# Kernel optimization log

Measured on AMD Instinct MI355X. Metric: run time of the kernel, lower is better.

## Reference

```python
import jax, jax.numpy as jnp
import numpy as np

D_MODEL = 256
D_INNER = 512
D_STATE = 16
DT_RANK = 16
D_CONV = 4
N_LAYERS = 2
EPS = 1e-5
SEQ_LEN = 16384
IN_DIM = 32
OUT_DIM = 1


def _layernorm(x, g, b):
    m = jnp.mean(x, axis=-1, keepdims=True)
    v = jnp.mean((x - m) ** 2, axis=-1, keepdims=True)
    return (x - m) * jax.lax.rsqrt(v + EPS) * g + b


def _rmsnorm(x, w):
    return x * jax.lax.rsqrt(jnp.mean(x * x, axis=-1, keepdims=True) + EPS) * w


def _selective_scan(x, delta, A, B, C, D):
    # x, delta: (B,L,ED); A: (ED,N); B,C: (B,L,N); D: (ED,)
    dA = jnp.exp(delta[..., None] * A)                    # (B,L,ED,N)
    dBx = (delta * x)[..., None] * B[:, :, None, :]       # (B,L,ED,N)

    def comb(l, r):
        al, bl = l
        ar, br = r
        return (al * ar, bl * ar + br)

    _, hs = jax.lax.associative_scan(comb, (dA, dBx), axis=1)  # (B,L,ED,N)
    y = jnp.einsum('blen,bln->ble', hs, C) + x * D
    return y


def _mamba_block(u, rms_w, inW, convW, convB, xpW, dtW, dtB, A_log, Dp, outW):
    h = _rmsnorm(u, rms_w)
    xz = h @ inW                                   # (B,L,2*ED)
    xin, z = jnp.split(xz, 2, axis=-1)
    # depthwise causal conv1d over time
    xc = jax.lax.conv_general_dilated(
        jnp.transpose(xin, (0, 2, 1)), convW,
        window_strides=(1,), padding=[(D_CONV - 1, 0)],
        feature_group_count=D_INNER,
        dimension_numbers=('NCH', 'OIH', 'NCH')) + convB[None, :, None]
    xs = jax.nn.silu(jnp.transpose(xc, (0, 2, 1)))  # (B,L,ED)
    dbc = xs @ xpW                                  # (B,L,dt_rank+2N)
    delta = jax.nn.softplus(dbc[..., :DT_RANK] @ dtW + dtB)
    Bm = dbc[..., DT_RANK:DT_RANK + D_STATE]
    Cm = dbc[..., DT_RANK + D_STATE:]
    y = _selective_scan(xs, delta, -jnp.exp(A_log), Bm, Cm, Dp)
    out = (y * jax.nn.silu(z)) @ outW
    return u + out  # residual


def _forward(x, W_in, b_in, ln1_g, ln1_b,
             rms_w, inW, convW, convB, xpW, dtW, dtB, A_log, Dp, outW,
             ln2_g, ln2_b, W1, b1, ln3_g, ln3_b, W2, b2):
    # input_proj (dropout = identity in eval)
    h = jax.nn.gelu(_layernorm(x[0] @ W_in + b_in, ln1_g, ln1_b))
    h = h[None]  # (1,L,D)
    for i in range(N_LAYERS):
        h = _mamba_block(h, rms_w[i], inW[i], convW[i], convB[i], xpW[i],
                         dtW[i], dtB[i], A_log[i], Dp[i], outW[i])
    # output_proj
    h = _layernorm(h, ln2_g, ln2_b)
    h = jax.nn.gelu(h @ W1 + b1)
    h = _layernorm(h, ln3_g, ln3_b)
    h = jnp.tanh(h @ W2 + b2)
    return h.reshape(-1)


def setup_inputs() -> dict:
    key = jax.random.key(0)
    ks = jax.random.split(key, 16)
    s = 0.02
    A = jnp.tile(jnp.arange(1, D_STATE + 1, dtype=jnp.float32)[None, :], (D_INNER, 1))
    return {
        'x': jax.random.normal(ks[0], (1, SEQ_LEN, IN_DIM), jnp.float32),
        'W_in': s * jax.random.normal(ks[1], (IN_DIM, D_MODEL), jnp.float32),
        'b_in': jnp.zeros((D_MODEL,), jnp.float32),
        'ln1_g': jnp.ones((D_MODEL,), jnp.float32),
        'ln1_b': jnp.zeros((D_MODEL,), jnp.float32),
        'rms_w': jnp.ones((N_LAYERS, D_MODEL), jnp.float32),
        'inW': s * jax.random.normal(ks[2], (N_LAYERS, D_MODEL, 2 * D_INNER), jnp.float32),
        'convW': s * jax.random.normal(ks[3], (N_LAYERS, D_INNER, 1, D_CONV), jnp.float32),
        'convB': jnp.zeros((N_LAYERS, D_INNER), jnp.float32),
        'xpW': s * jax.random.normal(ks[4], (N_LAYERS, D_INNER, DT_RANK + 2 * D_STATE), jnp.float32),
        'dtW': s * jax.random.normal(ks[5], (N_LAYERS, DT_RANK, D_INNER), jnp.float32),
        'dtB': 0.1 * jax.random.normal(ks[6], (N_LAYERS, D_INNER), jnp.float32),
        'A_log': jnp.tile(jnp.log(A)[None], (N_LAYERS, 1, 1)),
        'Dp': jnp.ones((N_LAYERS, D_INNER), jnp.float32),
        'outW': s * jax.random.normal(ks[7], (N_LAYERS, D_INNER, D_MODEL), jnp.float32),
        'ln2_g': jnp.ones((D_MODEL,), jnp.float32),
        'ln2_b': jnp.zeros((D_MODEL,), jnp.float32),
        'W1': s * jax.random.normal(ks[8], (D_MODEL, D_MODEL // 2), jnp.float32),
        'b1': jnp.zeros((D_MODEL // 2,), jnp.float32),
        'ln3_g': jnp.ones((D_MODEL // 2,), jnp.float32),
        'ln3_b': jnp.zeros((D_MODEL // 2,), jnp.float32),
        'W2': s * jax.random.normal(ks[9], (D_MODEL // 2, OUT_DIM), jnp.float32),
        'b2': jnp.zeros((OUT_DIM,), jnp.float32),
    }


def reference(x, W_in, b_in, ln1_g, ln1_b, rms_w, inW, convW, convB, xpW,
              dtW, dtB, A_log, Dp, outW, ln2_g, ln2_b, W1, b1, ln3_g, ln3_b,
              W2, b2):
    return _forward(x, W_in, b_in, ln1_g, ln1_b, rms_w, inW, convW, convB,
                    xpW, dtW, dtB, A_log, Dp, outW, ln2_g, ln2_b, W1, b1,
                    ln3_g, ln3_b, W2, b2)
```

## Files before the change

kernel.cpp:

```cpp
#include <hip/hip_runtime.h>
#include <hip/hip_bf16.h>
#include <math.h>

#define L_SEQ 16384
#define DM 256
#define DI 512
#define DS 16
#define NCH 512
#define CHL 32
#define CLB 16

typedef __attribute__((ext_vector_type(8))) short short8v;
typedef __attribute__((ext_vector_type(4))) float f32x4;

__device__ __forceinline__ float tanh_fast(float x){
  float xc = fminf(x, 15.f);
  float t = __expf(2.f*xc);
  return (t-1.f)/(t+1.f);
}
__device__ __forceinline__ float gelu_f(float x){
  float x3 = x*x*x;
  return 0.5f*x*(1.0f + tanh_fast(0.7978845608028654f*(x + 0.044715f*x3)));
}
__device__ __forceinline__ float silu_f(float x){
  return x / (1.0f + __expf(-x));
}
__device__ __forceinline__ float softplus_f(float x){
  return fmaxf(x,0.0f) + __logf(1.0f + __expf(-fabsf(x)));
}
__device__ __forceinline__ float bf2f(unsigned short u){
  return __uint_as_float(((unsigned int)u)<<16);
}
__device__ __forceinline__ void gload16(const void* g, void* l){
  __builtin_amdgcn_global_load_lds((const __attribute__((address_space(1))) void*)g,
                                   (__attribute__((address_space(3))) void*)l, 16, 0, 0);
}

__device__ __forceinline__ void powers16(float r, float* dA){
  float r2 = r*r;
  float r4 = r2*r2;
  float r8 = r4*r4;
  dA[0]=r;        dA[1]=r2;       dA[2]=r2*r;     dA[3]=r4;
  dA[4]=r4*r;     dA[5]=r4*r2;    dA[6]=r4*dA[2]; dA[7]=r8;
  dA[8]=r8*r;     dA[9]=r8*r2;    dA[10]=r8*dA[2];dA[11]=r8*r4;
  dA[12]=r8*dA[4];dA[13]=r8*dA[5];dA[14]=r8*dA[6];dA[15]=r8*r8;
}

__global__ void k_prep(const float* __restrict__ inW, const float* __restrict__ rmsw,
                       const float* __restrict__ outW, const float* __restrict__ W1,
                       const float* __restrict__ xpW, const float* __restrict__ dtW,
                       __hip_bfloat16* __restrict__ inWt, __hip_bfloat16* __restrict__ outWt,
                       __hip_bfloat16* __restrict__ W1t, __hip_bfloat16* __restrict__ Wdbc_t,
                       float* __restrict__ rowsq1){
  int idx = blockIdx.x*256 + threadIdx.x;
  if(idx < 524288){
    int layer = idx >> 18;
    int r = idx & 262143;
    int n = r >> 8, k = r & 255;
    inWt[idx] = __float2bfloat16(inW[layer*262144 + k*1024 + n] * rmsw[layer*256+k]);
  } else if(idx < 786432){
    int j = idx - 524288;
    int layer = j >> 17;
    int r = j & 131071;
    int n = r >> 9, k = r & 511;
    outWt[j] = __float2bfloat16(outW[layer*131072 + k*256 + n]);
  } else if(idx < 819200){
    int j = idx - 786432;
    int n = j >> 8, k = j & 255;
    W1t[j] = __float2bfloat16(W1[k*128 + n]);
  } else if(idx < 1474560){
    int j = idx - 819200;
    int layer = j / 327680;
    int r = j % 327680;
    int n = r >> 9, k = r & 511;
    const float* xp = xpW + layer*512*48;
    float v;
    if(n < 512){
      const float* dt = dtW + layer*16*512;
      float s = 0.f;
#pragma unroll
      for(int q=0;q<16;q++) s = fmaf(xp[k*48+q], dt[q*512+n], s);
      v = s;
    } else if(n < 544){
      v = xp[k*48 + 16 + (n-512)];
    } else v = 0.f;
    Wdbc_t[j] = __float2bfloat16(v);
  } else if(idx < 1490944){
    rowsq1[idx - 1474560] = 0.f;
  }
}

__global__ __launch_bounds__(256) void k_input(const float* __restrict__ x,
                        const float* __restrict__ Win, const float* __restrict__ bin,
                        const float* __restrict__ g, const float* __restrict__ b,
                        __hip_bfloat16* __restrict__ u, float* __restrict__ rowsq){
  int wv = threadIdx.x>>6, lane = threadIdx.x&63;
  int r = blockIdx.x*4 + wv;
  int c0 = lane*4;
  float acc[4];
  { float4 bv = *(const float4*)&bin[c0];
    acc[0]=bv.x; acc[1]=bv.y; acc[2]=bv.z; acc[3]=bv.w; }
#pragma unroll
  for(int k=0;k<32;k++){
    float xk = x[r*32+k];
    float4 wv4 = *(const float4*)&Win[k*DM+c0];
    acc[0]=fmaf(xk,wv4.x,acc[0]); acc[1]=fmaf(xk,wv4.y,acc[1]);
    acc[2]=fmaf(xk,wv4.z,acc[2]); acc[3]=fmaf(xk,wv4.w,acc[3]);
  }
  float s = (acc[0]+acc[1])+(acc[2]+acc[3]);
  float sq = acc[0]*acc[0]+acc[1]*acc[1]+acc[2]*acc[2]+acc[3]*acc[3];
#pragma unroll
  for(int o=32;o;o>>=1){ s += __shfl_xor(s,o); sq += __shfl_xor(sq,o); }
  float mean = s*(1.0f/DM);
  float var = sq*(1.0f/DM) - mean*mean;
  float rs = rsqrtf(var+1e-5f);
  float4 gv = *(const float4*)&g[c0];
  float4 bv = *(const float4*)&b[c0];
  float go[4];
  go[0] = gelu_f((acc[0]-mean)*rs*gv.x+bv.x);
  go[1] = gelu_f((acc[1]-mean)*rs*gv.y+bv.y);
  go[2] = gelu_f((acc[2]-mean)*rs*gv.z+bv.z);
  go[3] = gelu_f((acc[3]-mean)*rs*gv.w+bv.w);
  float ssq = go[0]*go[0]+go[1]*go[1]+go[2]*go[2]+go[3]*go[3];
#pragma unroll
  for(int o=32;o;o>>=1) ssq += __shfl_xor(ssq,o);
  if(lane==0) rowsq[r] = ssq;
  __hip_bfloat16 ob[4] = {__float2bfloat16(go[0]),__float2bfloat16(go[1]),
                          __float2bfloat16(go[2]),__float2bfloat16(go[3])};
  *(uint2*)&u[r*DM+c0] = *(uint2*)ob;
}

__global__ __launch_bounds__(256) void k_ln(const __hip_bfloat16* __restrict__ u,
                     const float* __restrict__ g, const float* __restrict__ b,
                     __hip_bfloat16* __restrict__ o){
  int wv = threadIdx.x>>6, lane = threadIdx.x&63;
  int r = blockIdx.x*4 + wv;
  int c0 = lane*4;
  ushort4 uv = *(const ushort4*)&u[r*DM+c0];
  float v[4] = {bf2f(uv.x), bf2f(uv.y), bf2f(uv.z), bf2f(uv.w)};
  float s = (v[0]+v[1])+(v[2]+v[3]);
  float sq = v[0]*v[0]+v[1]*v[1]+v[2]*v[2]+v[3]*v[3];
#pragma unroll
  for(int o2=32;o2;o2>>=1){ s += __shfl_xor(s,o2); sq += __shfl_xor(sq,o2); }
  float mean = s*(1.0f/DM);
  float var = sq*(1.0f/DM) - mean*mean;
  float rs = rsqrtf(var+1e-5f);
  float4 gv = *(const float4*)&g[c0];
  float4 bv = *(const float4*)&b[c0];
  __hip_bfloat16 ob[4] = {
    __float2bfloat16((v[0]-mean)*rs*gv.x+bv.x),
    __float2bfloat16((v[1]-mean)*rs*gv.y+bv.y),
    __float2bfloat16((v[2]-mean)*rs*gv.z+bv.z),
    __float2bfloat16((v[3]-mean)*rs*gv.w+bv.w)};
  *(uint2*)&o[r*DM+c0] = *(uint2*)ob;
}

template<int EPI, typename OT>
__global__ __launch_bounds__(512) void k_mgemm(const __hip_bfloat16* __restrict__ A,
    const __hip_bfloat16* __restrict__ Wt, const float* __restrict__ bias,
    const OT* __restrict__ R, OT* __restrict__ C, float* __restrict__ C2,
    float* __restrict__ rowsq, int M, int K, int ldc, int Nout){
  __shared__ char lds[66560];
  float* Ob = (float*)lds;
  int t = threadIdx.x, lane = t&63, wave = t>>6;
  int gx = gridDim.x;
  int f = blockIdx.y*gx + blockIdx.x;
  int s = f >> 3;
  int sy = s/gx;
  int yb = (f&7)*(gridDim.y>>3) + sy;
  int xb = s - sy*gx;
  int m0 = yb*128, n0 = xb*128;
  int wm = (wave>>1)*32, wn = (wave&1)*64;
  f32x4 acc[2][4] = {};
  int soff[2], srow[2], scol[2];
#pragma unroll
  for(int c=0;c<2;c++){
    int off = c*8192 + t*16;
    int row = off>>7;
    int sl  = ((off>>4)&7) ^ (row&7);
    soff[c]=off; srow[c]=row; scol[c]=sl*8;
  }
  int nk = K >> 6;
#pragma unroll
  for(int c=0;c<2;c++){
    gload16(&A [(m0+srow[c])*K + scol[c]], lds + soff[c]);
    gload16(&Wt[(n0+srow[c])*K + scol[c]], lds + 32768 + soff[c]);
  }
  for(int ki=0; ki<nk; ki++){
    int co = (ki & 1) ? 16384 : 0;
    if(ki+1 < nk){
      int no = co ^ 16384;
      int kt = (ki+1)<<6;
#pragma unroll
      for(int c=0;c<2;c++){
        gload16(&A [(m0+srow[c])*K + kt + scol[c]], lds + no + soff[c]);
        gload16(&Wt[(n0+srow[c])*K + kt + scol[c]], lds + 32768 + no + soff[c]);
      }
      asm volatile("s_waitcnt vmcnt(4)" ::: "memory");
    } else {
      asm volatile("s_waitcnt vmcnt(0)" ::: "memory");
    }
    __builtin_amdgcn_s_barrier();
    asm volatile("" ::: "memory");
    const short* As = (const short*)(lds + co);
    const short* Bs = (const short*)(lds + 32768 + co);
#pragma unroll
    for(int ks=0; ks<2; ks++){
      short8v a[2], b[4];
      int k8 = ks*4 + (lane>>4);
#pragma unroll
      for(int i=0;i<2;i++){
        int lr = wm + i*16 + (lane&15);
        a[i] = *(const short8v*)&As[lr*64 + (k8 ^ (lr&7))*8];
      }
#pragma unroll
      for(int j=0;j<4;j++){
        int lr = wn + j*16 + (lane&15);
        b[j] = *(const short8v*)&Bs[lr*64 + (k8 ^ (lr&7))*8];
      }
#pragma unroll
      for(int i=0;i<2;i++)
#pragma unroll
        for(int j=0;j<4;j++)
          acc[i][j] = __builtin_amdgcn_mfma_f32_16x16x32_bf16(a[i], b[j], acc[i][j], 0,0,0);
    }
    asm volatile("" ::: "memory");
    __builtin_amdgcn_s_barrier();
  }
#pragma unroll
  for(int h=0; h<2; h++){
    __syncthreads();
    if((wm>>6)==h){
      int base = wm & 63;
#pragma unroll
      for(int i=0;i<2;i++)
#pragma unroll
        for(int j=0;j<4;j++)
#pragma unroll
          for(int r=0;r<4;r++)
            Ob[(base + i*16 + (lane>>4)*4 + r)*132 + wn + j*16 + (lane&15)] = acc[i][j][r];
    }
    __syncthreads();
    float ssq_acc = 0.f;
#pragma unroll
    for(int v=0; v<4; v++){
      int fidx = (t*4+v)*4;
      int row = fidx>>7, col = fidx&127;
      if(col < Nout){
        float4 o = *(const float4*)&Ob[row*132 + col];
        int grow = m0 + h*64 + row, gcol = n0 + col;
        if(EPI==1 || EPI==5){
          if constexpr(sizeof(OT)==2){
            ushort4 rv = *(const ushort4*)&R[grow*ldc+gcol];
            o.x+=bf2f(rv.x); o.y+=bf2f(rv.y); o.z+=bf2f(rv.z); o.w+=bf2f(rv.w);
          } else {
            float4 rv = *(const float4*)&R[grow*ldc+gcol];
            o.x+=rv.x; o.y+=rv.y; o.z+=rv.z; o.w+=rv.w;
          }
          if(EPI==5) ssq_acc += o.x*o.x + o.y*o.y + o.z*o.z + o.w*o.w;
        }
        if(EPI==2){
          float4 bv = *(const float4*)&bias[gcol];
          o.x=gelu_f(o.x+bv.x); o.y=gelu_f(o.y+bv.y);
          o.z=gelu_f(o.z+bv.z); o.w=gelu_f(o.w+bv.w);
        }
        if(EPI==6){
          float rs = rsqrtf(rowsq[grow]*(1.0f/DM) + 1e-5f);
          o.x*=rs; o.y*=rs; o.z*=rs; o.w*=rs;
        }
        if(EPI==4){
          if(gcol < 512){
            float4 bv = *(const float4*)&bias[gcol];
            float4 so = {softplus_f(o.x+bv.x), softplus_f(o.y+bv.y),
                         softplus_f(o.z+bv.z), softplus_f(o.w+bv.w)};
            __hip_bfloat16 ob[4] = {__float2bfloat16(so.x),__float2bfloat16(so.y),
                                    __float2bfloat16(so.z),__float2bfloat16(so.w)};
            *(uint2*)&C[grow*ldc+gcol] = *(uint2*)ob;
          } else {
            *(float4*)&C2[grow*32 + (gcol-512)] = o;
          }
        } else {
          if constexpr(sizeof(OT)==2){
            __hip_bfloat16 ob[4] = {__float2bfloat16(o.x),__float2bfloat16(o.y),
                                    __float2bfloat16(o.z),__float2bfloat16(o.w)};
            *(uint2*)&C[grow*ldc+gcol] = *(uint2*)ob;
          } else {
            *(float4*)&C[grow*ldc+gcol] = o;
          }
        }
      }
    }
    if(EPI==5){
      ssq_acc += __shfl_xor(ssq_acc,1);
      ssq_acc += __shfl_xor(ssq_acc,2);
      ssq_acc += __shfl_xor(ssq_acc,4);
      if((t&7)==0) atomicAdd(&rowsq[m0 + h*64 + (t>>3)], ssq_acc);
    }
  }
}

__global__ __launch_bounds__(256) void k_conv(const __hip_bfloat16* __restrict__ xz,
                       const float* __restrict__ cw, const float* __restrict__ cb,
                       __hip_bfloat16* __restrict__ xs_bf){
  int idx = blockIdx.x*256 + threadIdx.x;
  int cg = idx & 127, lb = idx >> 7;
  int c4 = cg*4;
  int l0 = lb*CLB;
  float w[4][4], bias[4];
#pragma unroll
  for(int j=0;j<4;j++){
    float4 wv = *(const float4*)&cw[(c4+j)*4];
    w[j][0]=wv.x; w[j][1]=wv.y; w[j][2]=wv.z; w[j][3]=wv.w;
  }
  { float4 bv = *(const float4*)&cb[c4];
    bias[0]=bv.x; bias[1]=bv.y; bias[2]=bv.z; bias[3]=bv.w; }
  float xm0[4], xm1[4], xm2[4];
#pragma unroll
  for(int j=0;j<4;j++){ xm0[j]=0.f; xm1[j]=0.f; xm2[j]=0.f; }
  if(l0 >= 3){
    ushort4 r0 = *(const ushort4*)&xz[(l0-3)*1024 + c4];
    ushort4 r1 = *(const ushort4*)&xz[(l0-2)*1024 + c4];
    ushort4 r2 = *(const ushort4*)&xz[(l0-1)*1024 + c4];
    xm0[0]=bf2f(r0.x); xm0[1]=bf2f(r0.y); xm0[2]=bf2f(r0.z); xm0[3]=bf2f(r0.w);
    xm1[0]=bf2f(r1.x); xm1[1]=bf2f(r1.y); xm1[2]=bf2f(r1.z); xm1[3]=bf2f(r1.w);
    xm2[0]=bf2f(r2.x); xm2[1]=bf2f(r2.y); xm2[2]=bf2f(r2.z); xm2[3]=bf2f(r2.w);
  }
#pragma unroll 4
  for(int l=l0; l<l0+CLB; l++){
    ushort4 rc = *(const ushort4*)&xz[l*1024 + c4];
    float xc[4] = {bf2f(rc.x), bf2f(rc.y), bf2f(rc.z), bf2f(rc.w)};
    __hip_bfloat16 ob[4];
#pragma unroll
    for(int j=0;j<4;j++){
      float acc = bias[j];
      acc = fmaf(xm0[j], w[j][0], acc);
      acc = fmaf(xm1[j], w[j][1], acc);
      acc = fmaf(xm2[j], w[j][2], acc);
      acc = fmaf(xc[j],  w[j][3], acc);
      ob[j] = __float2bfloat16(silu_f(acc));
    }
    *(uint2*)&xs_bf[l*DI + c4] = *(uint2*)ob;
#pragma unroll
    for(int j=0;j<4;j++){ xm0[j]=xm1[j]; xm1[j]=xm2[j]; xm2[j]=xc[j]; }
  }
}

__global__ __launch_bounds__(256) void k_scan1(const __hip_bfloat16* __restrict__ delta,
                        const __hip_bfloat16* __restrict__ xs,
                        const float* __restrict__ dbc32, const float* __restrict__ A_log,
                        __hip_bfloat16* __restrict__ Atot, __hip_bfloat16* __restrict__ Btot){
  __shared__ float bcs[CHL*32];
  int t = threadIdx.x;
  int chunk = blockIdx.x >> 1;
  int e = ((blockIdx.x & 1) << 8) + t;
  int l0 = chunk*CHL;
  ((float4*)bcs)[t] = ((const float4*)&dbc32[l0*32])[t];
  float A[16];
  {
    const float4* al = (const float4*)&A_log[e*DS];
#pragma unroll
    for(int q=0;q<4;q++){
      float4 a = al[q];
      A[q*4+0] = -__expf(a.x); A[q*4+1] = -__expf(a.y);
      A[q*4+2] = -__expf(a.z); A[q*4+3] = -__expf(a.w);
    }
  }
  bool pf = true;
#pragma unroll
  for(int n=1;n<16;n++) pf = pf && (fabsf(A[n] - (n+1)*A[0]) <= 1e-4f*fabsf(A[n]));
  float carry[16], aprod[16];
#pragma unroll
  for(int n=0;n<16;n++){ carry[n]=0.f; aprod[n]=1.f; }
  __syncthreads();
  if(pf){
    float A0 = A[0];
#pragma unroll 2
    for(int li=0; li<CHL; li++){
      int l = l0 + li;
      float d  = bf2f(*(const unsigned short*)&delta[l*DI+e]);
      float xv = bf2f(*(const unsigned short*)&xs[l*DI+e]);
      float dxv = d*xv;
      const float4* bp = (const float4*)&bcs[li*32];
      float4 b0=bp[0], b1=bp[1], b2=bp[2], b3=bp[3];
      float B[16] = {b0.x,b0.y,b0.z,b0.w, b1.x,b1.y,b1.z,b1.w,
                     b2.x,b2.y,b2.z,b2.w, b3.x,b3.y,b3.z,b3.w};
      float r = __expf(d*A0);
      float dA[16]; powers16(r, dA);
#pragma unroll
      for(int n=0;n<16;n++){
        carry[n] = fmaf(carry[n], dA[n], dxv*B[n]);
        aprod[n] *= dA[n];
      }
    }
  } else {
#pragma unroll 2
    for(int li=0; li<CHL; li++){
      int l = l0 + li;
      float d  = bf2f(*(const unsigned short*)&delta[l*DI+e]);
      float xv = bf2f(*(const unsigned short*)&xs[l*DI+e]);
      float dxv = d*xv;
      const float4* bp = (const float4*)&bcs[li*32];
      float4 b0=bp[0], b1=bp[1], b2=bp[2], b3=bp[3];
      float B[16] = {b0.x,b0.y,b0.z,b0.w, b1.x,b1.y,b1.z,b1.w,
                     b2.x,b2.y,b2.z,b2.w, b3.x,b3.y,b3.z,b3.w};
#pragma unroll
      for(int n=0;n<16;n++){
        float dA = __expf(d*A[n]);
        carry[n] = fmaf(carry[n], dA, dxv*B[n]);
        aprod[n] *= dA;
      }
    }
  }
  __hip_bfloat16 apk[16], bpk[16];
#pragma unroll
  for(int n=0;n<16;n++){
    apk[n] = __float2bfloat16(aprod[n]);
    bpk[n] = __float2bfloat16(carry[n]);
  }
  uint4* ap = (uint4*)&Atot[chunk*8192 + e*DS];
  uint4* bp = (uint4*)&Btot[chunk*8192 + e*DS];
  ap[0] = ((const uint4*)apk)[0]; ap[1] = ((const uint4*)apk)[1];
  bp[0] = ((const uint4*)bpk)[0]; bp[1] = ((const uint4*)bpk)[1];
}

__global__ __launch_bounds__(64) void k_scan2(const __hip_bfloat16* __restrict__ Atot,
                        const __hip_bfloat16* __restrict__ Btot,
                        __hip_bfloat16* __restrict__ h0){
  int tg = blockIdx.x*64 + threadIdx.x;
  float carry = 0.f;
  for(int c0=0;c0<NCH;c0+=8){
    float a[8], b[8];
#pragma unroll
    for(int j=0;j<8;j++){
      a[j] = bf2f(*(const unsigned short*)&Atot[(c0+j)*8192+tg]);
      b[j] = bf2f(*(const unsigned short*)&Btot[(c0+j)*8192+tg]);
    }
#pragma unroll
    for(int j=0;j<8;j++){
      h0[(c0+j)*8192+tg] = __float2bfloat16(carry);
      carry = fmaf(carry, a[j], b[j]);
    }
  }
}

__global__ __launch_bounds__(256) void k_scan3(const __hip_bfloat16* __restrict__ delta,
                        const __hip_bfloat16* __restrict__ xs,
                        const float* __restrict__ dbc32, const float* __restrict__ A_log,
                        const float* __restrict__ Dp, const __hip_bfloat16* __restrict__ h0,
                        const __hip_bfloat16* __restrict__ xz, __hip_bfloat16* __restrict__ y){
  __shared__ float bcs[CHL*32];
  int t = threadIdx.x;
  int chunk = blockIdx.x >> 1;
  int e = ((blockIdx.x & 1) << 8) + t;
  int l0 = chunk*CHL;
  ((float4*)bcs)[t] = ((const float4*)&dbc32[l0*32])[t];
  float A[16];
  {
    const float4* al = (const float4*)&A_log[e*DS];
#pragma unroll
    for(int q=0;q<4;q++){
      float4 a = al[q];
      A[q*4+0] = -__expf(a.x); A[q*4+1] = -__expf(a.y);
      A[q*4+2] = -__expf(a.z); A[q*4+3] = -__expf(a.w);
    }
  }
  bool pf = true;
#pragma unroll
  for(int n=1;n<16;n++) pf = pf && (fabsf(A[n] - (n+1)*A[0]) <= 1e-4f*fabsf(A[n]));
  float carry[16];
  {
    uint4 h0a = ((const uint4*)&h0[chunk*8192 + e*DS])[0];
    uint4 h0b = ((const uint4*)&h0[chunk*8192 + e*DS])[1];
    const unsigned short* hp = (const unsigned short*)&h0a;
#pragma unroll
    for(int n=0;n<8;n++) carry[n] = bf2f(hp[n]);
    const unsigned short* hq = (const unsigned short*)&h0b;
#pragma unroll
    for(int n=0;n<8;n++) carry[8+n] = bf2f(hq[n]);
  }
  float Dv = Dp[e];
  __syncthreads();
  if(pf){
    float A0 = A[0];
#pragma unroll 2
    for(int li=0; li<CHL; li++){
      int l = l0 + li;
      float d  = bf2f(*(const unsigned short*)&delta[l*DI+e]);
      float xv = bf2f(*(const unsigned short*)&xs[l*DI+e]);
      float dxv = d*xv;
      const float4* bp = (const float4*)&bcs[li*32];
      float4 b0=bp[0], b1=bp[1], b2=bp[2], b3=bp[3];
      float4 c0=bp[4], c1=bp[5], c2=bp[6], c3=bp[7];
      float B[16] = {b0.x,b0.y,b0.z,b0.w, b1.x,b1.y,b1.z,b1.w,
                     b2.x,b2.y,b2.z,b2.w, b3.x,b3.y,b3.z,b3.w};
      float Cv[16] = {c0.x,c0.y,c0.z,c0.w, c1.x,c1.y,c1.z,c1.w,
                      c2.x,c2.y,c2.z,c2.w, c3.x,c3.y,c3.z,c3.w};
      float r = __expf(d*A0);
      float dA[16]; powers16(r, dA);
      float p[4] = {0.f,0.f,0.f,0.f};
#pragma unroll
      for(int n=0;n<16;n++){
        carry[n] = fmaf(carry[n], dA[n], dxv*B[n]);
        p[n&3] = fmaf(carry[n], Cv[n], p[n&3]);
      }
      float ps = (p[0]+p[1]) + (p[2]+p[3]);
      float z = bf2f(*(const unsigned short*)&xz[l*1024 + 512 + e]);
      y[l*DI+e] = __float2bfloat16(fmaf(xv, Dv, ps) * silu_f(z));
    }
  } else {
#pragma unroll 2
    for(int li=0; li<CHL; li++){
      int l = l0 + li;
      float d  = bf2f(*(const unsigned short*)&delta[l*DI+e]);
      float xv = bf2f(*(const unsigned short*)&xs[l*DI+e]);
      float dxv = d*xv;
      const float4* bp = (const float4*)&bcs[li*32];
      float4 b0=bp[0], b1=bp[1], b2=bp[2], b3=bp[3];
      float4 c0=bp[4], c1=bp[5], c2=bp[6], c3=bp[7];
      float B[16] = {b0.x,b0.y,b0.z,b0.w, b1.x,b1.y,b1.z,b1.w,
                     b2.x,b2.y,b2.z,b2.w, b3.x,b3.y,b3.z,b3.w};
      float Cv[16] = {c0.x,c0.y,c0.z,c0.w, c1.x,c1.y,c1.z,c1.w,
                      c2.x,c2.y,c2.z,c2.w, c3.x,c3.y,c3.z,c3.w};
      float p[4] = {0.f,0.f,0.f,0.f};
#pragma unroll
      for(int n=0;n<16;n++){
        float dA = __expf(d*A[n]);
        carry[n] = fmaf(carry[n], dA, dxv*B[n]);
        p[n&3] = fmaf(carry[n], Cv[n], p[n&3]);
      }
      float ps = (p[0]+p[1]) + (p[2]+p[3]);
      float z = bf2f(*(const unsigned short*)&xz[l*1024 + 512 + e]);
      y[l*DI+e] = __float2bfloat16(fmaf(xv, Dv, ps) * silu_f(z));
    }
  }
}

__global__ void k_final(const float* __restrict__ h2, const float* __restrict__ g,
                        const float* __restrict__ b, const float* __restrict__ W2,
                        const float* __restrict__ b2, float* __restrict__ out){
  int lane = threadIdx.x&63;
  int wv = threadIdx.x>>6;
  int r = blockIdx.x*4 + wv;
  float v0 = h2[r*128+lane], v1 = h2[r*128+64+lane];
  float s = v0+v1, sq = v0*v0+v1*v1;
#pragma unroll
  for(int o=32;o;o>>=1){ s += __shfl_xor(s,o); sq += __shfl_xor(sq,o); }
  float mean = s*(1.0f/128), var = sq*(1.0f/128) - mean*mean;
  float rs = rsqrtf(var+1e-5f);
  float n0 = (v0-mean)*rs*g[lane]+b[lane];
  float n1 = (v1-mean)*rs*g[lane+64]+b[lane+64];
  float d = n0*W2[lane] + n1*W2[lane+64];
#pragma unroll
  for(int o=32;o;o>>=1) d += __shfl_xor(d,o);
  if(lane==0) out[r] = tanhf(d + b2[0]);
}

extern "C" void kernel_launch(void* const* d_in, const int* in_sizes, int n_in,
                              void* d_out, int out_size, void* d_ws, size_t ws_size,
                              hipStream_t stream){
  const float* x    = (const float*)d_in[0];
  const float* Win  = (const float*)d_in[1];
  const float* bin  = (const float*)d_in[2];
  const float* ln1g = (const float*)d_in[3];
  const float* ln1b = (const float*)d_in[4];
  const float* rmsw = (const float*)d_in[5];
  const float* inW  = (const float*)d_in[6];
  const float* convW= (const float*)d_in[7];
  const float* convB= (const float*)d_in[8];
  const float* xpW  = (const float*)d_in[9];
  const float* dtW  = (const float*)d_in[10];
  const float* dtB  = (const float*)d_in[11];
  const float* A_log= (const float*)d_in[12];
  const float* Dp   = (const float*)d_in[13];
  const float* outW = (const float*)d_in[14];
  const float* ln2g = (const float*)d_in[15];
  const float* ln2b = (const float*)d_in[16];
  const float* W1   = (const float*)d_in[17];
  const float* b1   = (const float*)d_in[18];
  const float* ln3g = (const float*)d_in[19];
  const float* ln3b = (const float*)d_in[20];
  const float* W2   = (const float*)d_in[21];
  const float* b2   = (const float*)d_in[22];
  float* out = (float*)d_out;
  float* ws = (float*)d_ws;
  __hip_bfloat16* u_bf = (__hip_bfloat16*)ws;
  float* rowsq0 = ws + 4194304;
  float* rowsq1 = ws + 4210688;
  __hip_bfloat16* hn_bf = (__hip_bfloat16*)(ws + 4259840);
  __hip_bfloat16* xz_bf = (__hip_bfloat16*)(ws + 8388608);
  float* dbc32 = ws + 16777216;
  __hip_bfloat16* delta_bf = (__hip_bfloat16*)(ws + 17301504);
  __hip_bfloat16* y_bf  = (__hip_bfloat16*)(ws + 25690112);
  __hip_bfloat16* xs_bf = (__hip_bfloat16*)(ws + 29884416);
  __hip_bfloat16* Atot  = (__hip_bfloat16*)(ws + 34078720);
  __hip_bfloat16* Btot  = (__hip_bfloat16*)(ws + 36175872);
  __hip_bfloat16* h0    = Btot;
  float* h2    = ws;
  __hip_bfloat16* inWt   = (__hip_bfloat16*)(ws + 42467328);
  __hip_bfloat16* outWt  = (__hip_bfloat16*)(ws + 42729472);
  __hip_bfloat16* W1t    = (__hip_bfloat16*)(ws + 42860544);
  __hip_bfloat16* Wdbc_t = (__hip_bfloat16*)(ws + 42876928);

  k_prep<<<5824,256,0,stream>>>(inW, rmsw, outW, W1, xpW, dtW, inWt, outWt, W1t, Wdbc_t, rowsq1);
  k_input<<<L_SEQ/4,256,0,stream>>>(x,Win,bin,ln1g,ln1b,u_bf,rowsq0);
  for(int i=0;i<2;i++){
    float* rsq_in = (i==0) ? rowsq0 : rowsq1;
    k_mgemm<6,__hip_bfloat16><<<dim3(8, L_SEQ/128),512,0,stream>>>(
        u_bf, inWt+i*262144, nullptr, nullptr, xz_bf, nullptr, rsq_in, L_SEQ, DM, 1024, 1024);
    k_conv<<<(L_SEQ/CLB)*128/256,256,0,stream>>>(xz_bf, convW+i*DI*4, convB+i*DI, xs_bf);
    k_mgemm<4,__hip_bfloat16><<<dim3(5, L_SEQ/128),512,0,stream>>>(
        xs_bf, Wdbc_t+i*327680, dtB+i*DI, nullptr, delta_bf, dbc32, nullptr, L_SEQ, DI, 512, 544);
    k_scan1<<<NCH*2,256,0,stream>>>(delta_bf, xs_bf, dbc32, A_log+i*DI*DS, Atot, Btot);
    k_scan2<<<128,64,0,stream>>>(Atot, Btot, h0);
    k_scan3<<<NCH*2,256,0,stream>>>(delta_bf, xs_bf, dbc32, A_log+i*DI*DS, Dp+i*DI, h0, xz_bf, y_bf);
    if(i==0){
      k_mgemm<5,__hip_bfloat16><<<dim3(2, L_SEQ/128),512,0,stream>>>(
          y_bf, outWt, nullptr, u_bf, u_bf, nullptr, rowsq1, L_SEQ, DI, 256, 256);
    } else {
      k_mgemm<1,__hip_bfloat16><<<dim3(2, L_SEQ/128),512,0,stream>>>(
          y_bf, outWt+131072, nullptr, u_bf, u_bf, nullptr, nullptr, L_SEQ, DI, 256, 256);
    }
  }
  k_ln<<<L_SEQ/4,256,0,stream>>>(u_bf, ln2g, ln2b, hn_bf);
  k_mgemm<2,float><<<dim3(1, L_SEQ/128),512,0,stream>>>(
      hn_bf, W1t, b1, nullptr, h2, nullptr, nullptr, L_SEQ, DM, 128, 128);
  k_final<<<L_SEQ/4,256,0,stream>>>(h2, ln3g, ln3b, W2, b2, out);
}
```

Baseline: 357.7 us.

## Fold final LayerNorm into W1 GEMM and fuse output head into epilogue

The ln2 gamma is folded into W1, and the ln2 beta/bias terms are precomputed into a parameter vector. Row sums and sums of squares are accumulated atomically in the last out-projection epilogue, so the standalone LayerNorm kernel is removed. The W1 GEMM now reads the residual stream directly and applies mean/rstd, GELU, LN3, the W2 dot and tanh in its epilogue, which eliminates the k_ln and k_final launches and the h2/hn intermediates. The trade-offs are extra atomics and changed numerics: variance is computed from bf16-rounded sums, and the folded weights are quantized to bf16.

```diff
diff --git a/kernel.cpp b/kernel.cpp
--- a/kernel.cpp
+++ b/kernel.cpp
@@ -49,9 +49,14 @@
 __global__ void k_prep(const float* __restrict__ inW, const float* __restrict__ rmsw,
                        const float* __restrict__ outW, const float* __restrict__ W1,
                        const float* __restrict__ xpW, const float* __restrict__ dtW,
+                       const float* __restrict__ ln2g, const float* __restrict__ ln2b,
+                       const float* __restrict__ b1, const float* __restrict__ ln3g,
+                       const float* __restrict__ ln3b, const float* __restrict__ W2,
+                       const float* __restrict__ b2,
                        __hip_bfloat16* __restrict__ inWt, __hip_bfloat16* __restrict__ outWt,
                        __hip_bfloat16* __restrict__ W1t, __hip_bfloat16* __restrict__ Wdbc_t,
-                       float* __restrict__ rowsq1){
+                       float* __restrict__ rowsq1, float* __restrict__ rowsum2,
+                       float* __restrict__ rowsq2, float* __restrict__ pars){
   int idx = blockIdx.x*256 + threadIdx.x;
   if(idx < 524288){
     int layer = idx >> 18;
@@ -67,7 +72,7 @@
   } else if(idx < 819200){
     int j = idx - 786432;
     int n = j >> 8, k = j & 255;
-    W1t[j] = __float2bfloat16(W1[k*128 + n]);
+    W1t[j] = __float2bfloat16(W1[k*128 + n] * ln2g[k]);
   } else if(idx < 1474560){
     int j = idx - 819200;
     int layer = j / 327680;
@@ -87,6 +92,25 @@
     Wdbc_t[j] = __float2bfloat16(v);
   } else if(idx < 1490944){
     rowsq1[idx - 1474560] = 0.f;
+  } else if(idx < 1507328){
+    rowsum2[idx - 1490944] = 0.f;
+  } else if(idx < 1523712){
+    rowsq2[idx - 1507328] = 0.f;
+  } else if(idx < 1524353){
+    int j = idx - 1523712;
+    if(j < 128){
+      float s = 0.f;
+      for(int k=0;k<256;k++) s = fmaf(ln2g[k], W1[k*128+j], s);
+      pars[j] = s;
+    } else if(j < 256){
+      int n = j - 128;
+      float s = 0.f;
+      for(int k=0;k<256;k++) s = fmaf(ln2b[k], W1[k*128+n], s);
+      pars[j] = s + b1[n];
+    } else if(j < 384) pars[j] = ln3g[j-256];
+    else if(j < 512)   pars[j] = ln3b[j-384];
+    else if(j < 640)   pars[j] = W2[j-512];
+    else               pars[640] = b2[0];
   }
 }
 
@@ -128,31 +152,6 @@
   __hip_bfloat16 ob[4] = {__float2bfloat16(go[0]),__float2bfloat16(go[1]),
                           __float2bfloat16(go[2]),__float2bfloat16(go[3])};
   *(uint2*)&u[r*DM+c0] = *(uint2*)ob;
-}
-
-__global__ __launch_bounds__(256) void k_ln(const __hip_bfloat16* __restrict__ u,
-                     const float* __restrict__ g, const float* __restrict__ b,
-                     __hip_bfloat16* __restrict__ o){
-  int wv = threadIdx.x>>6, lane = threadIdx.x&63;
-  int r = blockIdx.x*4 + wv;
-  int c0 = lane*4;
-  ushort4 uv = *(const ushort4*)&u[r*DM+c0];
-  float v[4] = {bf2f(uv.x), bf2f(uv.y), bf2f(uv.z), bf2f(uv.w)};
-  float s = (v[0]+v[1])+(v[2]+v[3]);
-  float sq = v[0]*v[0]+v[1]*v[1]+v[2]*v[2]+v[3]*v[3];
-#pragma unroll
-  for(int o2=32;o2;o2>>=1){ s += __shfl_xor(s,o2); sq += __shfl_xor(sq,o2); }
-  float mean = s*(1.0f/DM);
-  float var = sq*(1.0f/DM) - mean*mean;
-  float rs = rsqrtf(var+1e-5f);
-  float4 gv = *(const float4*)&g[c0];
-  float4 bv = *(const float4*)&b[c0];
-  __hip_bfloat16 ob[4] = {
-    __float2bfloat16((v[0]-mean)*rs*gv.x+bv.x),
-    __float2bfloat16((v[1]-mean)*rs*gv.y+bv.y),
-    __float2bfloat16((v[2]-mean)*rs*gv.z+bv.z),
-    __float2bfloat16((v[3]-mean)*rs*gv.w+bv.w)};
-  *(uint2*)&o[r*DM+c0] = *(uint2*)ob;
 }
 
 template<int EPI, typename OT>
@@ -241,60 +240,99 @@
             Ob[(base + i*16 + (lane>>4)*4 + r)*132 + wn + j*16 + (lane&15)] = acc[i][j][r];
     }
     __syncthreads();
-    float ssq_acc = 0.f;
-#pragma unroll
-    for(int v=0; v<4; v++){
-      int fidx = (t*4+v)*4;
-      int row = fidx>>7, col = fidx&127;
-      if(col < Nout){
-        float4 o = *(const float4*)&Ob[row*132 + col];
-        int grow = m0 + h*64 + row, gcol = n0 + col;
-        if(EPI==1 || EPI==5){
-          if constexpr(sizeof(OT)==2){
-            ushort4 rv = *(const ushort4*)&R[grow*ldc+gcol];
-            o.x+=bf2f(rv.x); o.y+=bf2f(rv.y); o.z+=bf2f(rv.z); o.w+=bf2f(rv.w);
+    if constexpr(EPI==8){
+      int rl = t>>3;
+      int grow = m0 + h*64 + rl;
+      int c0b = (t&7)*16;
+      float mean = (float)R[grow]*(1.0f/DM);
+      float var = rowsq[grow]*(1.0f/DM) - mean*mean;
+      float rsv = rsqrtf(var+1e-5f);
+      float hbuf[16];
+      float s3=0.f, q3=0.f;
+#pragma unroll
+      for(int v=0;v<4;v++){
+        float4 o = *(const float4*)&Ob[rl*132 + c0b + v*4];
+        float oa[4] = {o.x,o.y,o.z,o.w};
+#pragma unroll
+        for(int j=0;j<4;j++){
+          int col = c0b + v*4 + j;
+          float val = rsv*oa[j] - rsv*mean*C2[col] + C2[128+col];
+          float hh = gelu_f(val);
+          hbuf[v*4+j] = hh;
+          s3 += hh; q3 += hh*hh;
+        }
+      }
+      s3 += __shfl_xor(s3,1); q3 += __shfl_xor(q3,1);
+      s3 += __shfl_xor(s3,2); q3 += __shfl_xor(q3,2);
+      s3 += __shfl_xor(s3,4); q3 += __shfl_xor(q3,4);
+      float m3 = s3*(1.0f/128), v3 = q3*(1.0f/128) - m3*m3;
+      float rs3 = rsqrtf(v3+1e-5f);
+      float dot = 0.f;
+#pragma unroll
+      for(int j=0;j<16;j++){
+        int col = c0b + j;
+        dot += ((hbuf[j]-m3)*rs3*C2[256+col] + C2[384+col]) * C2[512+col];
+      }
+      dot += __shfl_xor(dot,1); dot += __shfl_xor(dot,2); dot += __shfl_xor(dot,4);
+      if((t&7)==0) C[grow] = tanh_fast(dot + C2[640]);
+    } else {
+      float ssq_acc = 0.f, ssum_acc = 0.f;
+#pragma unroll
+      for(int v=0; v<4; v++){
+        int fidx = (t*4+v)*4;
+        int row = fidx>>7, col = fidx&127;
+        if(col < Nout){
+          float4 o = *(const float4*)&Ob[row*132 + col];
+          int grow = m0 + h*64 + row, gcol = n0 + col;
+          if(EPI==1 || EPI==5 || EPI==7){
+            if constexpr(sizeof(OT)==2){
+              ushort4 rv = *(const ushort4*)&R[grow*ldc+gcol];
+              o.x+=bf2f(rv.x); o.y+=bf2f(rv.y); o.z+=bf2f(rv.z); o.w+=bf2f(rv.w);
+            } else {
+              float4 rv = *(const float4*)&R[grow*ldc+gcol];
+              o.x+=rv.x; o.y+=rv.y; o.z+=rv.z; o.w+=rv.w;
+            }
+            if(EPI==5 || EPI==7) ssq_acc += o.x*o.x + o.y*o.y + o.z*o.z + o.w*o.w;
+            if(EPI==7) ssum_acc += o.x + o.y + o.z + o.w;
+          }
+          if(EPI==6){
+            float rs = rsqrtf(rowsq[grow]*(1.0f/DM) + 1e-5f);
+            o.x*=rs; o.y*=rs; o.z*=rs; o.w*=rs;
+          }
+          if(EPI==4){
+            if(gcol < 512){
+              float4 bv = *(const float4*)&bias[gcol];
+              float4 so = {softplus_f(o.x+bv.x), softplus_f(o.y+bv.y),
+                           softplus_f(o.z+bv.z), softplus_f(o.w+bv.w)};
+              __hip_bfloat16 ob[4] = {__float2bfloat16(so.x),__float2bfloat16(so.y),
+                                      __float2bfloat16(so.z),__float2bfloat16(so.w)};
+              *(uint2*)&C[grow*ldc+gcol] = *(uint2*)ob;
+            } else {
+              *(float4*)&C2[grow*32 + (gcol-512)] = o;
+            }
           } else {
-            float4 rv = *(const float4*)&R[grow*ldc+gcol];
-            o.x+=rv.x; o.y+=rv.y; o.z+=rv.z; o.w+=rv.w;
-          }
-          if(EPI==5) ssq_acc += o.x*o.x + o.y*o.y + o.z*o.z + o.w*o.w;
-        }
-        if(EPI==2){
-          float4 bv = *(const float4*)&bias[gcol];
-          o.x=gelu_f(o.x+bv.x); o.y=gelu_f(o.y+bv.y);
-          o.z=gelu_f(o.z+bv.z); o.w=gelu_f(o.w+bv.w);
-        }
-        if(EPI==6){
-          float rs = rsqrtf(rowsq[grow]*(1.0f/DM) + 1e-5f);
-          o.x*=rs; o.y*=rs; o.z*=rs; o.w*=rs;
-        }
-        if(EPI==4){
-          if(gcol < 512){
-            float4 bv = *(const float4*)&bias[gcol];
-            float4 so = {softplus_f(o.x+bv.x), softplus_f(o.y+bv.y),
-                         softplus_f(o.z+bv.z), softplus_f(o.w+bv.w)};
-            __hip_bfloat16 ob[4] = {__float2bfloat16(so.x),__float2bfloat16(so.y),
-                                    __float2bfloat16(so.z),__float2bfloat16(so.w)};
-            *(uint2*)&C[grow*ldc+gcol] = *(uint2*)ob;
-          } else {
-            *(float4*)&C2[grow*32 + (gcol-512)] = o;
-          }
-        } else {
-          if constexpr(sizeof(OT)==2){
-            __hip_bfloat16 ob[4] = {__float2bfloat16(o.x),__float2bfloat16(o.y),
-                                    __float2bfloat16(o.z),__float2bfloat16(o.w)};
-            *(uint2*)&C[grow*ldc+gcol] = *(uint2*)ob;
-          } else {
-            *(float4*)&C[grow*ldc+gcol] = o;
+            if constexpr(sizeof(OT)==2){
+              __hip_bfloat16 ob[4] = {__float2bfloat16(o.x),__float2bfloat16(o.y),
+                                      __float2bfloat16(o.z),__float2bfloat16(o.w)};
+              *(uint2*)&C[grow*ldc+gcol] = *(uint2*)ob;
+            } else {
+              *(float4*)&C[grow*ldc+gcol] = o;
+            }
           }
         }
       }
-    }
-    if(EPI==5){
-      ssq_acc += __shfl_xor(ssq_acc,1);
-      ssq_acc += __shfl_xor(ssq_acc,2);
-      ssq_acc += __shfl_xor(ssq_acc,4);
-      if((t&7)==0) atomicAdd(&rowsq[m0 + h*64 + (t>>3)], ssq_acc);
+      if(EPI==5 || EPI==7){
+        ssq_acc += __shfl_xor(ssq_acc,1);
+        ssq_acc += __shfl_xor(ssq_acc,2);
+        ssq_acc += __shfl_xor(ssq_acc,4);
+        if((t&7)==0) atomicAdd(&rowsq[m0 + h*64 + (t>>3)], ssq_acc);
+      }
+      if(EPI==7){
+        ssum_acc += __shfl_xor(ssum_acc,1);
+        ssum_acc += __shfl_xor(ssum_acc,2);
+        ssum_acc += __shfl_xor(ssum_acc,4);
+        if((t&7)==0) atomicAdd(&C2[m0 + h*64 + (t>>3)], ssum_acc);
+      }
     }
   }
 }
@@ -533,26 +571,6 @@
       y[l*DI+e] = __float2bfloat16(fmaf(xv, Dv, ps) * silu_f(z));
     }
   }
-}
-
-__global__ void k_final(const float* __restrict__ h2, const float* __restrict__ g,
-                        const float* __restrict__ b, const float* __restrict__ W2,
-                        const float* __restrict__ b2, float* __restrict__ out){
-  int lane = threadIdx.x&63;
-  int wv = threadIdx.x>>6;
-  int r = blockIdx.x*4 + wv;
-  float v0 = h2[r*128+lane], v1 = h2[r*128+64+lane];
-  float s = v0+v1, sq = v0*v0+v1*v1;
-#pragma unroll
-  for(int o=32;o;o>>=1){ s += __shfl_xor(s,o); sq += __shfl_xor(sq,o); }
-  float mean = s*(1.0f/128), var = sq*(1.0f/128) - mean*mean;
-  float rs = rsqrtf(var+1e-5f);
-  float n0 = (v0-mean)*rs*g[lane]+b[lane];
-  float n1 = (v1-mean)*rs*g[lane+64]+b[lane+64];
-  float d = n0*W2[lane] + n1*W2[lane+64];
-#pragma unroll
-  for(int o=32;o;o>>=1) d += __shfl_xor(d,o);
-  if(lane==0) out[r] = tanhf(d + b2[0]);
 }
 
 extern "C" void kernel_launch(void* const* d_in, const int* in_sizes, int n_in,
@@ -584,9 +602,11 @@
   float* out = (float*)d_out;
   float* ws = (float*)d_ws;
   __hip_bfloat16* u_bf = (__hip_bfloat16*)ws;
-  float* rowsq0 = ws + 4194304;
-  float* rowsq1 = ws + 4210688;
-  __hip_bfloat16* hn_bf = (__hip_bfloat16*)(ws + 4259840);
+  float* rowsq0  = ws + 4194304;
+  float* rowsq1  = ws + 4210688;
+  float* rowsum2 = ws + 4227072;
+  float* rowsq2  = ws + 4243456;
+  float* mlp_pars= ws + 4259840;
   __hip_bfloat16* xz_bf = (__hip_bfloat16*)(ws + 8388608);
   float* dbc32 = ws + 16777216;
   __hip_bfloat16* delta_bf = (__hip_bfloat16*)(ws + 17301504);
@@ -595,13 +615,14 @@
   __hip_bfloat16* Atot  = (__hip_bfloat16*)(ws + 34078720);
   __hip_bfloat16* Btot  = (__hip_bfloat16*)(ws + 36175872);
   __hip_bfloat16* h0    = Btot;
-  float* h2    = ws;
   __hip_bfloat16* inWt   = (__hip_bfloat16*)(ws + 42467328);
   __hip_bfloat16* outWt  = (__hip_bfloat16*)(ws + 42729472);
   __hip_bfloat16* W1t    = (__hip_bfloat16*)(ws + 42860544);
   __hip_bfloat16* Wdbc_t = (__hip_bfloat16*)(ws + 42876928);
 
-  k_prep<<<5824,256,0,stream>>>(inW, rmsw, outW, W1, xpW, dtW, inWt, outWt, W1t, Wdbc_t, rowsq1);
+  k_prep<<<5955,256,0,stream>>>(inW, rmsw, outW, W1, xpW, dtW, ln2g, ln2b, b1,
+                                ln3g, ln3b, W2, b2, inWt, outWt, W1t, Wdbc_t,
+                                rowsq1, rowsum2, rowsq2, mlp_pars);
   k_input<<<L_SEQ/4,256,0,stream>>>(x,Win,bin,ln1g,ln1b,u_bf,rowsq0);
   for(int i=0;i<2;i++){
     float* rsq_in = (i==0) ? rowsq0 : rowsq1;
@@ -617,12 +638,10 @@
       k_mgemm<5,__hip_bfloat16><<<dim3(2, L_SEQ/128),512,0,stream>>>(
           y_bf, outWt, nullptr, u_bf, u_bf, nullptr, rowsq1, L_SEQ, DI, 256, 256);
     } else {
-      k_mgemm<1,__hip_bfloat16><<<dim3(2, L_SEQ/128),512,0,stream>>>(
-          y_bf, outWt+131072, nullptr, u_bf, u_bf, nullptr, nullptr, L_SEQ, DI, 256, 256);
-    }
-  }
-  k_ln<<<L_SEQ/4,256,0,stream>>>(u_bf, ln2g, ln2b, hn_bf);
-  k_mgemm<2,float><<<dim3(1, L_SEQ/128),512,0,stream>>>(
-      hn_bf, W1t, b1, nullptr, h2, nullptr, nullptr, L_SEQ, DM, 128, 128);
-  k_final<<<L_SEQ/4,256,0,stream>>>(h2, ln3g, ln3b, W2, b2, out);
-}
+      k_mgemm<7,__hip_bfloat16><<<dim3(2, L_SEQ/128),512,0,stream>>>(
+          y_bf, outWt+131072, nullptr, u_bf, u_bf, rowsum2, rowsq2, L_SEQ, DI, 256, 256);
+    }
+  }
+  k_mgemm<8,float><<<dim3(1, L_SEQ/128),512,0,stream>>>(
+      u_bf, W1t, nullptr, rowsum2, out, mlp_pars, rowsq2, L_SEQ, DM, 128, 128);
+}
```

New measurement: 358.2 us. No clear change (+0.1%).
